# Kernel optimization log

Hardware: AMD Instinct MI355X
Metric: run time of the kernel (lower is better)

Reference implementation:

```python
import jax, jax.numpy as jnp
import numpy as np
from jax import lax

B, NQ, C = 2, 1024, 2048
H, DH = 16, 128
G, CD = 4, 512          # off_grps, off_dim = C // G
LR, HR = 24, 72         # low-res grid side, high-res grid side
INTER = 64
K = LR * LR             # sampled K/V tokens (grid_size == lr_size)


def setup_inputs() -> dict:
    key = jax.random.key(0)
    ks = jax.random.split(key, 16)
    s = 0.02
    d = {}
    d['hidden_states'] = jax.random.normal(ks[0], (B, NQ, C), jnp.float32)
    d['image_hd'] = jax.random.normal(ks[1], (B, HR * HR, C), jnp.float32)
    d['wq'] = jax.random.normal(ks[2], (C, C), jnp.float32) * s
    d['wk'] = jax.random.normal(ks[3], (C, C), jnp.float32) * s
    d['wv'] = jax.random.normal(ks[4], (C, C), jnp.float32) * s
    d['wo'] = jax.random.normal(ks[5], (C, C), jnp.float32) * s
    d['conv_dw_w'] = jax.random.normal(ks[6], (CD, 1, 3, 3), jnp.float32) * s
    d['ln1_w'] = jnp.ones((CD,), jnp.float32)
    d['ln1_b'] = jnp.zeros((CD,), jnp.float32)
    d['conv_lr_proj_w'] = jax.random.normal(ks[7], (INTER, CD), jnp.float32) * s
    d['proj_int_w'] = jax.random.normal(ks[8], (INTER, CD), jnp.float32) * s
    d['proj_int_b'] = jnp.zeros((INTER,), jnp.float32)
    d['ln2_w'] = jnp.ones((INTER,), jnp.float32)
    d['ln2_b'] = jnp.zeros((INTER,), jnp.float32)
    d['conv_off_w'] = jax.random.normal(ks[9], (2, INTER), jnp.float32) * s
    d['k_hd_w'] = jax.random.normal(ks[10], (C, C), jnp.float32) * s
    d['k_hd_b'] = jnp.zeros((C,), jnp.float32)
    d['v_hd_w'] = jax.random.normal(ks[11], (C, C), jnp.float32) * s
    d['v_hd_b'] = jnp.zeros((C,), jnp.float32)
    return d


def _ln_channels(x, w, b, eps=1e-5):
    # LayerNorm2d: normalize over channel axis of [N, C, H, W]
    mu = jnp.mean(x, axis=1, keepdims=True)
    var = jnp.var(x, axis=1, keepdims=True)
    xn = (x - mu) * lax.rsqrt(var + eps)
    return xn * w[None, :, None, None] + b[None, :, None, None]


def _tokens_to_grid(x, S):
    # [B, S*S, C] -> [B*G, CD, S, S]  (group channels like einops '(b) (h w) (g c) -> (b g) c h w')
    return x.reshape(B, S, S, G, CD).transpose(0, 3, 4, 1, 2).reshape(B * G, CD, S, S)


def _bilinear_sample(img, grid):
    # img [N, C, Hh, Wh]; grid [N, K, 2] (x, y) normalized to [-1, 1], align_corners=True
    N, Cc, Hh, Wh = img.shape
    x = (grid[..., 0] + 1.0) * 0.5 * (Wh - 1)
    y = (grid[..., 1] + 1.0) * 0.5 * (Hh - 1)
    x0f, y0f = jnp.floor(x), jnp.floor(y)
    wx = (x - x0f)[:, None, :]
    wy = (y - y0f)[:, None, :]
    x0 = jnp.clip(x0f.astype(jnp.int32), 0, Wh - 1)
    x1 = jnp.clip(x0 + 1, 0, Wh - 1)
    y0 = jnp.clip(y0f.astype(jnp.int32), 0, Hh - 1)
    y1 = jnp.clip(y0 + 1, 0, Hh - 1)
    imgf = img.reshape(N, Cc, Hh * Wh)
    gather = jax.vmap(lambda im, ix: im[:, ix])  # ([C,HW],[K]) -> [C,K]
    v00 = gather(imgf, y0 * Wh + x0)
    v01 = gather(imgf, y0 * Wh + x1)
    v10 = gather(imgf, y1 * Wh + x0)
    v11 = gather(imgf, y1 * Wh + x1)
    return (v00 * (1 - wx) * (1 - wy) + v01 * wx * (1 - wy)
            + v10 * (1 - wx) * wy + v11 * wx * wy)  # [N, C, K]


def _ref_grid():
    # normalized reference points as in _grid_generate (centers / (S-1) * 2 - 1)
    yy = (jnp.linspace(0.5, LR - 0.5, LR) / (LR - 1.0)) * 2.0 - 1.0
    xx = (jnp.linspace(0.5, LR - 0.5, LR) / (LR - 1.0)) * 2.0 - 1.0
    gy, gx = jnp.meshgrid(yy, xx, indexing='ij')
    return jnp.stack([gx, gy], axis=-1).reshape(K, 2)  # (x, y)


def reference(hidden_states, image_hd, wq, wk, wv, wo, conv_dw_w, ln1_w, ln1_b,
              conv_lr_proj_w, proj_int_w, proj_int_b, ln2_w, ln2_b, conv_off_w,
              k_hd_w, k_hd_b, v_hd_w, v_hd_b):
    # ---- QKV on the full sequence ----
    q = hidden_states @ wq.T
    k_txt = hidden_states @ wk.T
    v_txt = hidden_states @ wv.T

    # ---- offset network on LR image tokens (first LR*LR tokens) ----
    lr = _tokens_to_grid(hidden_states[:, :K, :], LR)          # [B*G, CD, LR, LR]
    x = lax.conv_general_dilated(lr, conv_dw_w, (1, 1), 'SAME',
                                 feature_group_count=CD,
                                 dimension_numbers=('NCHW', 'OIHW', 'NCHW'))
    x = jax.nn.silu(x)
    x = _ln_channels(x, ln1_w, ln1_b)
    x = jnp.einsum('nchw,oc->nohw', x, conv_lr_proj_w)          # 1x1 conv -> [B*G, INTER, LR, LR]
    # intention gate from spatially pooled group features
    pooled = jnp.mean(lr, axis=(2, 3))                          # [B*G, CD]
    gate = jax.nn.sigmoid(pooled @ proj_int_w.T + proj_int_b)   # [B*G, INTER]
    x = x * gate[:, :, None, None]
    x = _ln_channels(x, ln2_w, ln2_b)
    off = jnp.einsum('nchw,oc->nohw', x, conv_off_w)            # [B*G, 2, LR, LR]
    off = off.transpose(0, 2, 3, 1).reshape(B * G, K, 2)        # (x, y)
    pos = jnp.tanh(_ref_grid()[None] + off)                     # sampling locs in [-1, 1]

    # ---- deformable gather from HD features ----
    hd = _tokens_to_grid(image_hd, HR)                          # [B*G, CD, HR, HR]
    samp = _bilinear_sample(hd, pos)                            # [B*G, CD, K]
    samp = samp.reshape(B, G, CD, K).transpose(0, 3, 1, 2).reshape(B, K, C)
    k_hd = samp @ k_hd_w.T + k_hd_b
    v_hd = samp @ v_hd_w.T + v_hd_b

    # ---- attention: causal over text tokens, HD tokens fully visible ----
    k_all = jnp.concatenate([k_txt, k_hd], axis=1)              # [B, NQ+K, C]
    v_all = jnp.concatenate([v_txt, v_hd], axis=1)
    qh = q.reshape(B, NQ, H, DH).transpose(0, 2, 1, 3)
    kh = k_all.reshape(B, NQ + K, H, DH).transpose(0, 2, 1, 3)
    vh = v_all.reshape(B, NQ + K, H, DH).transpose(0, 2, 1, 3)
    scores = jnp.einsum('bhqd,bhkd->bhqk', qh, kh) / jnp.sqrt(jnp.float32(DH))
    col = jnp.arange(NQ + K)
    row = jnp.arange(NQ)
    allow = (col[None, :] >= NQ) | (col[None, :] <= row[:, None])
    scores = jnp.where(allow[None, None], scores, jnp.float32(-1e9))
    attn = jax.nn.softmax(scores, axis=-1)
    out = jnp.einsum('bhqk,bhkd->bhqd', attn, vh)
    out = out.transpose(0, 2, 1, 3).reshape(B, NQ, C)
    return out @ wo.T
```

## Files before the change

### kernel.cpp

```cpp
#include <hip/hip_runtime.h>

typedef unsigned short u16;
typedef unsigned int u32;
typedef __attribute__((ext_vector_type(8))) short bf8;
typedef __attribute__((ext_vector_type(4))) float f4;
typedef __attribute__((ext_vector_type(4))) unsigned short us4;

constexpr int B = 2;
constexpr int NQ = 1024;
constexpr int C = 2048;
constexpr int DH = 128;
constexpr int G = 4;
constexpr int CD = 512;
constexpr int LR = 24;
constexpr int HR = 72;
constexpr int INTER = 64;
constexpr int K = LR * LR;
constexpr int NKV = NQ + K;

#define MFMA16(a, b, c) __builtin_amdgcn_mfma_f32_16x16x32_bf16(a, b, c, 0, 0, 0)
#define GLDS(g, l)                                                         \
  __builtin_amdgcn_global_load_lds(                                        \
      (const __attribute__((address_space(1))) void*)(g),                  \
      (__attribute__((address_space(3))) void*)(l), 16, 0, 0)

__device__ __forceinline__ u16 f2bf1(float f) {
  u32 u = __float_as_uint(f);
  u32 r = (u + 0x7fffu + ((u >> 16) & 1u)) >> 16;
  return (u16)r;
}

__global__ __launch_bounds__(256) void f2bf_k7(
    const float* __restrict__ s0, const float* __restrict__ s1,
    const float* __restrict__ s2, const float* __restrict__ s3,
    const float* __restrict__ s4, const float* __restrict__ s5,
    const float* __restrict__ s6, u16* __restrict__ d0, u16* __restrict__ d1,
    u16* __restrict__ d2, u16* __restrict__ d3, u16* __restrict__ d4,
    u16* __restrict__ d5, u16* __restrict__ d6) {
  __shared__ u16 L[64][68];
  const int y = blockIdx.y;
  const float* s;
  u16* d;
  switch (y) {
    case 0: s = s0; d = d0; break;
    case 1: s = s1; d = d1; break;
    case 2: s = s2; d = d2; break;
    case 3: s = s3; d = d3; break;
    case 4: s = s4; d = d4; break;
    case 5: s = s5; d = d5; break;
    default: s = s6; d = d6; break;
  }
  const int t = threadIdx.x;
  if (y < 4) {
    const int pc = blockIdx.x;
    const int mb = pc >> 5, kb = pc & 31;
    const int rin = t >> 2, c0 = (t & 3) * 16;
    const float* src = s + (size_t)(mb * 64 + rin) * 2048 + kb * 64 + c0;
#pragma unroll
    for (int j = 0; j < 16; j += 4) {
      float4 v = *(const float4*)(src + j);
      L[rin][c0 + j] = f2bf1(v.x);
      L[rin][c0 + j + 1] = f2bf1(v.y);
      L[rin][c0 + j + 2] = f2bf1(v.z);
      L[rin][c0 + j + 3] = f2bf1(v.w);
    }
    __syncthreads();
    u16* dst = d + (size_t)pc * 4096 + t * 16;
#pragma unroll
    for (int gg = 0; gg < 2; ++gg) {
      const int g = t * 2 + gg;
      const int rh = g & 15, ks2 = (g >> 4) & 3, kc = (g >> 6) & 1, fr = g >> 7;
      const int row = fr * 16 + rh, cc = kc * 32 + ks2 * 8;
      us4 o0, o1;
      o0.x = L[row][cc];     o0.y = L[row][cc + 1];
      o0.z = L[row][cc + 2]; o0.w = L[row][cc + 3];
      o1.x = L[row][cc + 4]; o1.y = L[row][cc + 5];
      o1.z = L[row][cc + 6]; o1.w = L[row][cc + 7];
      *(us4*)(dst + gg * 8) = o0;
      *(us4*)(dst + gg * 8 + 4) = o1;
    }
  } else {
    const size_t i0 = ((size_t)blockIdx.x * 256 + t) * 16;
#pragma unroll
    for (int j = 0; j < 16; j += 4) {
      float4 v = *(const float4*)(s + i0 + j);
      us4 o;
      o.x = f2bf1(v.x); o.y = f2bf1(v.y); o.z = f2bf1(v.z); o.w = f2bf1(v.w);
      *(us4*)(d + i0 + j) = o;
    }
  }
}

#define SB()                               \
  do {                                     \
    __builtin_amdgcn_sched_barrier(0);     \
    __builtin_amdgcn_s_barrier();          \
    __builtin_amdgcn_sched_barrier(0);     \
  } while (0)
#define WVM(n) asm volatile("s_waitcnt vmcnt(" #n ")" ::: "memory")

__global__ __launch_bounds__(512, 2) void gemm_fused(
    const u16* __restrict__ Ast, const u16* __restrict__ Wq,
    const u16* __restrict__ Wk, const u16* __restrict__ Wv,
    const u16* __restrict__ samp, const u16* __restrict__ khw,
    const u16* __restrict__ vhw, const float* __restrict__ khb,
    const float* __restrict__ vhb, u16* __restrict__ outq,
    u16* __restrict__ kg, u16* __restrict__ vg) {
  __shared__ u16 As[2][4][4096];
  __shared__ u16 Bs[2][4][4096];
  const int tid = threadIdx.x, lane = tid & 63, w = tid >> 6;
  const int ks = lane >> 4, r = lane & 15;
  const int bid = blockIdx.x;

  if (bid < 192) {
    const int wm = w >> 2, wn = w & 3;
    const int swz = (bid & 7) * 24 + (bid >> 3);
    const int mt = swz / 24, nt = swz % 24;
    const u16* Wst = (nt < 8) ? Wq : (nt < 16) ? Wk : Wv;
    const int nb0 = (nt & 7) * 4;
    const int mb0 = mt * 4;

#define ST_A03(bi, kt)                                                        \
  do {                                                                        \
    GLDS(Ast + ((size_t)(mb0 + 0) * 32 + (kt)) * 4096 + tid * 8,              \
         &As[bi][0][tid * 8]);                                                \
    GLDS(Ast + ((size_t)(mb0 + 2) * 32 + (kt)) * 4096 + tid * 8,              \
         &As[bi][2][tid * 8]);                                                \
  } while (0)
#define ST_A47(bi, kt)                                                        \
  do {                                                                        \
    GLDS(Ast + ((size_t)(mb0 + 1) * 32 + (kt)) * 4096 + tid * 8,              \
         &As[bi][1][tid * 8]);                                                \
    GLDS(Ast + ((size_t)(mb0 + 3) * 32 + (kt)) * 4096 + tid * 8,              \
         &As[bi][3][tid * 8]);                                                \
  } while (0)
#define ST_B01(bi, kt)                                                        \
  do {                                                                        \
    GLDS(Wst + ((size_t)(nb0 + 0) * 32 + (kt)) * 4096 + tid * 8,              \
         &Bs[bi][0][tid * 8]);                                                \
    GLDS(Wst + ((size_t)(nb0 + 1) * 32 + (kt)) * 4096 + tid * 8,              \
         &Bs[bi][1][tid * 8]);                                                \
  } while (0)
#define ST_B23(bi, kt)                                                        \
  do {                                                                        \
    GLDS(Wst + ((size_t)(nb0 + 2) * 32 + (kt)) * 4096 + tid * 8,              \
         &Bs[bi][2][tid * 8]);                                                \
    GLDS(Wst + ((size_t)(nb0 + 3) * 32 + (kt)) * 4096 + tid * 8,              \
         &Bs[bi][3][tid * 8]);                                                \
  } while (0)
#define RD_A(dst, bi, half, kc)                                               \
  _Pragma("unroll") for (int i2 = 0; i2 < 4; ++i2) dst[i2] =                  \
      *(const bf8*)(&As[bi][wm * 2 + (half)]                                  \
                       [((i2 * 2 + (kc)) * 4 + ks) * 128 + r * 8]);
#define RD_B(dst, bi, kc)                                                     \
  _Pragma("unroll") for (int j2 = 0; j2 < 4; ++j2) dst[j2] =                  \
      *(const bf8*)(&Bs[bi][wn][((j2 * 2 + (kc)) * 4 + ks) * 128 + r * 8]);
#define MM(ACC, AF, BF)                                                       \
  do {                                                                        \
    __builtin_amdgcn_s_setprio(1);                                            \
    _Pragma("unroll") for (int i3 = 0; i3 < 4; ++i3)                          \
        _Pragma("unroll") for (int j3 = 0; j3 < 4; ++j3) ACC[i3][j3] =        \
            MFMA16(AF[i3], BF[j3], ACC[i3][j3]);                              \
    __builtin_amdgcn_s_setprio(0);                                            \
  } while (0)

    f4 accA[4][4], accB[4][4];
#pragma unroll
    for (int i = 0; i < 4; ++i)
#pragma unroll
      for (int j = 0; j < 4; ++j) {
        accA[i][j] = f4{0.f, 0.f, 0.f, 0.f};
        accB[i][j] = f4{0.f, 0.f, 0.f, 0.f};
      }
    bf8 af[4], b0[4], b1[4];

    ST_A03(0, 0); ST_B01(0, 0); ST_B23(0, 0); ST_A47(0, 0);
    ST_A03(1, 1); ST_B01(1, 1);
    WVM(6);
    SB();

    for (int t = 0; t < 32; ++t) {
      const int buf = t & 1;
      RD_A(af, buf, 0, 0);
      RD_B(b0, buf, 0);
      if (t + 1 < 32) ST_B23(buf ^ 1, t + 1);
      SB();
      MM(accA, af, b0);
      SB();
      RD_A(af, buf, 0, 1);
      RD_B(b1, buf, 1);
      if (t + 1 < 32) ST_A47(buf ^ 1, t + 1);
      SB();
      MM(accA, af, b1);
      if (t + 1 < 32) { WVM(8); } else { WVM(0); }
      SB();
      RD_A(af, buf, 1, 0);
      if (t + 2 < 32) ST_A03(buf, t + 2);
      SB();
      MM(accB, af, b0);
      SB();
      RD_A(af, buf, 1, 1);
      if (t + 2 < 32) ST_B01(buf, t + 2);
      SB();
      MM(accB, af, b1);
      if (t + 2 < 32) { WVM(6); } else if (t + 1 < 32) { WVM(2); }
      SB();
    }

#define EPI(ACC, HALF)                                                        \
  _Pragma("unroll") for (int i = 0; i < 4; ++i)                               \
      _Pragma("unroll") for (int j = 0; j < 4; ++j)                           \
          _Pragma("unroll") for (int rr = 0; rr < 4; ++rr) {                  \
    const int m = mt * 256 + wm * 128 + (HALF)*64 + i * 16 + ks * 4 + rr;     \
    const int n = nt * 256 + wn * 64 + j * 16 + r;                            \
    const float v = ACC[i][j][rr];                                            \
    const int sel = n >> 11, nn = n & 2047, hh = nn >> 7, dd = nn & 127;      \
    const int bb = m >> 10, qq = m & 1023;                                    \
    const u16 bv = f2bf1(v);                                                  \
    if (sel == 0) {                                                           \
      outq[(size_t)m * 2048 + nn] = bv;                                       \
    } else if (sel == 1) {                                                    \
      kg[(((size_t)(bb * 16 + hh) * 50 + (qq >> 5)) * 16 + (dd >> 3)) * 256 + \
         (qq & 31) * 8 + (dd & 7)] = bv;                                      \
    } else {                                                                  \
      vg[((size_t)(bb * 16 + hh) * 200 + (qq >> 3)) * 1024 + dd * 8 +         \
         (qq & 7)] = bv;                                                      \
    }                                                                         \
  }
    EPI(accA, 0)
    EPI(accB, 1)
#undef EPI
  } else {
    const int hb = bid - 192;
    const int mt = hb >> 4, nb = hb & 15;
    const int m0 = mt * 128, n0l = nb * 128;
    const int srow = lane >> 2, scol = (lane & 3) * 8;
    const int wh = w & 3;
    const int wr = wh >> 1, wc = wh & 1;
    const bool is_v = (w >= 4);
    const u16* Wp = is_v ? vhw : khw;
    const float* bias = is_v ? vhb : khb;

#define HDST(bi, k0)                                                          \
  do {                                                                        \
    GLDS(samp + (size_t)(m0 + w * 16 + srow) * 2048 + scol + (k0),            \
         &As[bi][0][w * 512 + lane * 8]);                                     \
    GLDS(Wp + (size_t)(n0l + wh * 32 + srow) * 2048 + scol + (k0),            \
         &Bs[bi][is_v ? 1 : 0][wh * 1024 + lane * 8]);                        \
    GLDS(Wp + (size_t)(n0l + wh * 32 + 16 + srow) * 2048 + scol + (k0),       \
         &Bs[bi][is_v ? 1 : 0][wh * 1024 + 512 + lane * 8]);                  \
  } while (0)

    f4 acc[4][4];
#pragma unroll
    for (int i = 0; i < 4; ++i)
#pragma unroll
      for (int j = 0; j < 4; ++j) acc[i][j] = f4{0.f, 0.f, 0.f, 0.f};
    const int koff = ks * 8;
    const int arow = wr * 64 + r, brow = wc * 64 + r;
    const u16* Wsb = &Bs[0][is_v ? 1 : 0][0] - 0;

    HDST(0, 0);
    int cur = 0;
    for (int k0 = 0; k0 < 2048; k0 += 32) {
      __syncthreads();
      if (k0 + 32 < 2048) HDST(cur ^ 1, k0 + 32);
      bf8 af2[4], bw[4];
#pragma unroll
      for (int i = 0; i < 4; ++i)
        af2[i] = *(const bf8*)(&As[cur][0][(arow + i * 16) * 32 + koff]);
#pragma unroll
      for (int j = 0; j < 4; ++j)
        bw[j] =
            *(const bf8*)(&Bs[cur][is_v ? 1 : 0][(brow + j * 16) * 32 + koff]);
#pragma unroll
      for (int i = 0; i < 4; ++i)
#pragma unroll
        for (int j = 0; j < 4; ++j)
          acc[i][j] = MFMA16(af2[i], bw[j], acc[i][j]);
      cur ^= 1;
    }
#undef HDST
    const int rbase = ks * 4;
#pragma unroll
    for (int i = 0; i < 4; ++i) {
#pragma unroll
      for (int j = 0; j < 4; ++j) {
        const int nn = n0l + wc * 64 + j * 16 + r;
        const int hh = nn >> 7, dd = nn & 127;
#pragma unroll
        for (int rr = 0; rr < 4; ++rr) {
          const int m = m0 + wr * 64 + i * 16 + rbase + rr;
          const int bb = m / 576;
          const int kv = 1024 + (m - bb * 576);
          const u16 bv = f2bf1(acc[i][j][rr] + bias[nn]);
          if (!is_v) {
            kg[(((size_t)(bb * 16 + hh) * 50 + (kv >> 5)) * 16 + (dd >> 3)) *
                   256 +
               (kv & 31) * 8 + (dd & 7)] = bv;
          } else {
            vg[((size_t)(bb * 16 + hh) * 200 + (kv >> 3)) * 1024 + dd * 8 +
               (kv & 7)] = bv;
          }
        }
      }
    }
  }
}

__global__ __launch_bounds__(256) void gemm_out(const u16* __restrict__ A,
                                                const u16* __restrict__ W0,
                                                float* __restrict__ outf) {
  __shared__ u16 As2[2][4096];
  __shared__ u16 Ws2[2][4096];
  const int tid = threadIdx.x, lane = tid & 63, w = tid >> 6;
  const int wr = w >> 1, wc = w & 1;
  const int m0 = blockIdx.y * 128, nb = blockIdx.x;
  const int n0l = nb * 128;
  f4 acc[4][4];
#pragma unroll
  for (int i = 0; i < 4; ++i)
#pragma unroll
    for (int j = 0; j < 4; ++j) acc[i][j] = f4{0.f, 0.f, 0.f, 0.f};
  const int srow = lane >> 2, scol = (lane & 3) * 8;
  const int ch0 = w * 2;
  const u16* Ab = A + (size_t)m0 * 2048 + scol;
  const u16* Wb = W0 + (size_t)n0l * 2048 + scol;
  const int koff = (lane >> 4) * 8;
  const int arow = wr * 64 + (lane & 15), brow = wc * 64 + (lane & 15);

#define GSTAGE(bi, k0)                                                        \
  do {                                                                        \
    _Pragma("unroll") for (int c = 0; c < 2; ++c) {                           \
      const int chunk = ch0 + c;                                              \
      const int row = chunk * 16 + srow;                                      \
      GLDS(Ab + (size_t)row * 2048 + (k0), &As2[bi][chunk * 512 + lane * 8]); \
      GLDS(Wb + (size_t)row * 2048 + (k0), &Ws2[bi][chunk * 512 + lane * 8]); \
    }                                                                         \
  } while (0)

  GSTAGE(0, 0);
  int cur = 0;
  for (int k0 = 0; k0 < 2048; k0 += 32) {
    __syncthreads();
    if (k0 + 32 < 2048) GSTAGE(cur ^ 1, k0 + 32);
    bf8 af2[4], bw[4];
#pragma unroll
    for (int i = 0; i < 4; ++i)
      af2[i] = *(const bf8*)(&As2[cur][(arow + i * 16) * 32 + koff]);
#pragma unroll
    for (int j = 0; j < 4; ++j)
      bw[j] = *(const bf8*)(&Ws2[cur][(brow + j * 16) * 32 + koff]);
#pragma unroll
    for (int i = 0; i < 4; ++i)
#pragma unroll
      for (int j = 0; j < 4; ++j)
        acc[i][j] = MFMA16(af2[i], bw[j], acc[i][j]);
    cur ^= 1;
  }
#undef GSTAGE
  const int rbase = (lane >> 4) * 4;
  const int cql = lane & 15;
#pragma unroll
  for (int i = 0; i < 4; ++i)
#pragma unroll
    for (int j = 0; j < 4; ++j) {
      const int n = n0l + wc * 64 + j * 16 + cql;
#pragma unroll
      for (int rr = 0; rr < 4; ++rr) {
        const int m = m0 + wr * 64 + i * 16 + rbase + rr;
        outf[(size_t)m * 2048 + n] = acc[i][j][rr];
      }
    }
}

__global__ __launch_bounds__(256) void build_lr_t(const float* __restrict__ hs,
                                                  float* __restrict__ lr) {
  __shared__ float L[32][65];
  const int bidx = blockIdx.x;
  const int n = bidx / 144;
  const int rem = bidx % 144;
  const int pb = rem / 16, cb = rem % 16;
  const int b = n >> 2, g = n & 3;
  const int p0 = pb * 64, c0 = cb * 32;
  const int t = threadIdx.x;
  const int cl = t & 31, pr = t >> 5;
#pragma unroll
  for (int it = 0; it < 8; ++it) {
    const int p = p0 + it * 8 + pr;
    L[cl][it * 8 + pr] =
        hs[((size_t)(b * 1024 + p)) * 2048 + g * 512 + c0 + cl];
  }
  __syncthreads();
  const int pl = t & 63, cr = t >> 6;
#pragma unroll
  for (int jt = 0; jt < 8; ++jt) {
    const int c = jt * 4 + cr;
    lr[((size_t)(n * 512) + c0 + c) * 576 + p0 + pl] = L[c][pl];
  }
}

__global__ __launch_bounds__(256) void pool_lr(const float* __restrict__ lr,
                                               float* __restrict__ pooled) {
  int row = (blockIdx.x * 256 + threadIdx.x) >> 6;
  int lane = threadIdx.x & 63;
  if (row >= B * G * CD) return;
  const float* p = lr + (size_t)row * K;
  float s = 0.f;
  for (int i = lane; i < K; i += 64) s += p[i];
  for (int o = 32; o; o >>= 1) s += __shfl_xor(s, o);
  if (lane == 0) pooled[row] = s * (1.f / K);
}

__global__ __launch_bounds__(256) void dwconv_silu(const float* __restrict__ lr,
                                                   const float* __restrict__ w,
                                                   float* __restrict__ x1) {
  int idx = blockIdx.x * 256 + threadIdx.x;
  if (idx >= B * G * CD * K) return;
  int p = idx % K;
  int c = (idx / K) % CD;
  int n = idx / (K * CD);
  int y = p / LR, x = p % LR;
  const float* wp = w + c * 9;
  const float* src = lr + ((size_t)n * CD + c) * K;
  float s = 0.f;
#pragma unroll
  for (int dy = -1; dy <= 1; ++dy)
#pragma unroll
    for (int dx = -1; dx <= 1; ++dx) {
      int yy = y + dy, xx = x + dx;
      if (yy < 0 || yy >= LR || xx < 0 || xx >= LR) continue;
      s += src[yy * LR + xx] * wp[(dy + 1) * 3 + dx + 1];
    }
  x1[idx] = s / (1.f + expf(-s));
}

__global__ __launch_bounds__(256) void ln_c512(float* __restrict__ x,
                                               const float* __restrict__ w,
                                               const float* __restrict__ b) {
  const int n = blockIdx.x / 9;
  const int p0 = (blockIdx.x % 9) * 64;
  const int pl = threadIdx.x & 63;
  const int cg = threadIdx.x >> 6;
  float* base = x + (size_t)n * CD * K + p0 + pl;
  float s = 0.f, ss = 0.f;
  for (int c = cg * 128; c < cg * 128 + 128; ++c) {
    float v = base[(size_t)c * K];
    s += v; ss += v * v;
  }
  __shared__ float rs[4][64], rss[4][64];
  rs[cg][pl] = s; rss[cg][pl] = ss;
  __syncthreads();
  float S = rs[0][pl] + rs[1][pl] + rs[2][pl] + rs[3][pl];
  float SS = rss[0][pl] + rss[1][pl] + rss[2][pl] + rss[3][pl];
  const float mean = S * (1.f / CD);
  const float inv = rsqrtf(SS * (1.f / CD) - mean * mean + 1e-5f);
  for (int c = cg * 128; c < cg * 128 + 128; ++c) {
    float v = base[(size_t)c * K];
    base[(size_t)c * K] = (v - mean) * inv * w[c] + b[c];
  }
}

__global__ __launch_bounds__(576) void proj64(const float* __restrict__ x1,
                                              const float* __restrict__ w,
                                              float* __restrict__ x2) {
  const int n = blockIdx.x >> 3;
  const int o0 = (blockIdx.x & 7) * 8;
  const int p = threadIdx.x;
  const float* xb = x1 + (size_t)n * CD * K + p;
  float acc[8] = {0.f, 0.f, 0.f, 0.f, 0.f, 0.f, 0.f, 0.f};
  for (int c = 0; c < CD; ++c) {
    float v = xb[(size_t)c * K];
#pragma unroll
    for (int j = 0; j < 8; ++j) acc[j] += v * w[(o0 + j) * CD + c];
  }
#pragma unroll
  for (int j = 0; j < 8; ++j)
    x2[((size_t)n * INTER + o0 + j) * K + p] = acc[j];
}

__global__ __launch_bounds__(64) void gate_k(const float* __restrict__ pooled,
                                             const float* __restrict__ w,
                                             const float* __restrict__ bias,
                                             float* __restrict__ gate) {
  int idx = blockIdx.x * 64 + threadIdx.x;
  if (idx >= B * G * INTER) return;
  int n = idx >> 6, o = idx & 63;
  const float* pb = pooled + n * CD;
  const float* wb = w + o * CD;
  float s = bias[o];
  for (int c = 0; c < CD; ++c) s += pb[c] * wb[c];
  gate[idx] = 1.f / (1.f + expf(-s));
}

__global__ __launch_bounds__(256) void ln2_off_pos(
    const float* __restrict__ x2, const float* __restrict__ gate,
    const float* __restrict__ ln2w, const float* __restrict__ ln2b,
    const float* __restrict__ offw, float* __restrict__ pos) {
  int wid = (blockIdx.x * 256 + threadIdx.x) >> 6;
  int lane = threadIdx.x & 63;
  if (wid >= B * G * K) return;
  int n = wid / K, p = wid % K;
  float v = x2[((size_t)n * INTER + lane) * K + p] * gate[n * INTER + lane];
  float s = v, ss = v * v;
  for (int o = 32; o; o >>= 1) {
    s += __shfl_xor(s, o);
    ss += __shfl_xor(ss, o);
  }
  float mean = s * (1.f / INTER);
  float var = ss * (1.f / INTER) - mean * mean;
  float xn = (v - mean) * rsqrtf(var + 1e-5f) * ln2w[lane] + ln2b[lane];
  float ox = xn * offw[lane];
  float oy = xn * offw[INTER + lane];
  for (int o = 32; o; o >>= 1) {
    ox += __shfl_xor(ox, o);
    oy += __shfl_xor(oy, o);
  }
  if (lane == 0) {
    int yi = p / LR, xi = p % LR;
    float rx = (xi + 0.5f) / 23.f * 2.f - 1.f;
    float ry = (yi + 0.5f) / 23.f * 2.f - 1.f;
    pos[((size_t)n * K + p) * 2 + 0] = tanhf(rx + ox);
    pos[((size_t)n * K + p) * 2 + 1] = tanhf(ry + oy);
  }
}

__global__ __launch_bounds__(256) void sample_k(const float* __restrict__ img,
                                                const float* __restrict__ pos,
                                                u16* __restrict__ samp) {
  const int bk = blockIdx.x;
  const int b = bk / K, k = bk % K;
  __shared__ int s_idx[G][4];
  __shared__ float s_w[G][4];
  if (threadIdx.x < G) {
    int g = threadIdx.x;
    int n = b * G + g;
    float px = pos[((size_t)n * K + k) * 2 + 0];
    float py = pos[((size_t)n * K + k) * 2 + 1];
    float x = (px + 1.f) * 0.5f * (HR - 1);
    float y = (py + 1.f) * 0.5f * (HR - 1);
    float x0f = floorf(x), y0f = floorf(y);
    float wx = x - x0f, wy = y - y0f;
    int x0 = min(max((int)x0f, 0), HR - 1);
    int x1 = min(x0 + 1, HR - 1);
    int y0 = min(max((int)y0f, 0), HR - 1);
    int y1 = min(y0 + 1, HR - 1);
    s_idx[g][0] = y0 * HR + x0;
    s_idx[g][1] = y0 * HR + x1;
    s_idx[g][2] = y1 * HR + x0;
    s_idx[g][3] = y1 * HR + x1;
    s_w[g][0] = (1.f - wx) * (1.f - wy);
    s_w[g][1] = wx * (1.f - wy);
    s_w[g][2] = (1.f - wx) * wy;
    s_w[g][3] = wx * wy;
  }
  __syncthreads();
  const float* ib = img + (size_t)b * HR * HR * C;
  u16* ob = samp + ((size_t)b * K + k) * C;
  for (int ch = threadIdx.x; ch < C; ch += 256) {
    int g = ch >> 9;
    float v = s_w[g][0] * ib[(size_t)s_idx[g][0] * C + ch] +
              s_w[g][1] * ib[(size_t)s_idx[g][1] * C + ch] +
              s_w[g][2] * ib[(size_t)s_idx[g][2] * C + ch] +
              s_w[g][3] * ib[(size_t)s_idx[g][3] * C + ch];
    ob[ch] = f2bf1(v);
  }
}

__global__ __launch_bounds__(256) void attn_part(
    const u16* __restrict__ qb, const u16* __restrict__ kg,
    const u16* __restrict__ vg, float* __restrict__ oA,
    float* __restrict__ oB, float* __restrict__ mlA,
    float* __restrict__ mlB) {
  const int i = blockIdx.x;
  const int fam = i >> 9;
  const int r9 = i & 511;
  int bh, qblk;
  if (fam == 0) {
    const int pair = r9 & 255, half = r9 >> 8;
    bh = pair & 31;
    const int q8 = pair >> 5;
    qblk = half ? (15 - q8) : q8;
  } else {
    bh = r9 & 31;
    qblk = r9 >> 5;
  }
  const int b = bh >> 4, h = bh & 15;
  const int q0 = qblk * 64;
  const int tid = threadIdx.x, lane = tid & 63, w = tid >> 6;
  const int qw = q0 + w * 16;
  const int col = lane & 15, kpart = lane >> 4, rbase = kpart * 4;
  __shared__ u16 Ks[2][4096];
  __shared__ u16 Vs[2][4096];
  __shared__ u16 Pl[4][16 * 40];
  float* oacc = fam ? oB : oA;
  float* ml = fam ? mlB : mlA;
  bf8 qf[4];
  {
    const u16* qp =
        qb + (size_t)(b * 1024 + qw + col) * 2048 + h * 128 + kpart * 8;
#pragma unroll
    for (int dc = 0; dc < 4; ++dc) qf[dc] = *(const bf8*)(qp + dc * 32);
  }
  f4 o[8];
#pragma unroll
  for (int df = 0; df < 8; ++df) o[df] = f4{0.f, 0.f, 0.f, 0.f};
  float m_r[4] = {-1e30f, -1e30f, -1e30f, -1e30f};
  float l_p[4] = {0.f, 0.f, 0.f, 0.f};
  const float scale = 0.08838834764831845f;
  const int nt = fam ? 18 : ((q0 + 64) >> 5);
  const int kvadd = fam ? 1024 : 0;
  const u16* kbh = kg + (size_t)bh * (NKV * 128);
  const u16* vbh = vg + (size_t)bh * (NKV * 128);
  u16* pw = &Pl[w][0];

#define ASTAGE(bi, kv0)                                                       \
  do {                                                                        \
    const u16* gk = kbh + (size_t)((kv0) >> 5) * 4096 + w * 1024 + lane * 8;  \
    GLDS(gk, &Ks[bi][w * 1024 + lane * 8]);                                   \
    GLDS(gk + 512, &Ks[bi][w * 1024 + 512 + lane * 8]);                       \
    const u16* gv = vbh + (size_t)((kv0) >> 3) * 1024 + w * 1024 + lane * 8;  \
    GLDS(gv, &Vs[bi][w * 1024 + lane * 8]);                                   \
    GLDS(gv + 512, &Vs[bi][w * 1024 + 512 + lane * 8]);                       \
  } while (0)

  ASTAGE(0, kvadd);
  int cur = 0;
  for (int t = 0; t < nt; ++t) {
    const int kv0 = kvadd + (t << 5);
    __syncthreads();
    if (t + 1 < nt) ASTAGE(cur ^ 1, kvadd + ((t + 1) << 5));
    const u16* ksb = &Ks[cur][0];
    const u16* vsb = &Vs[cur][0];
    f4 s0 = {0.f, 0.f, 0.f, 0.f}, s1 = {0.f, 0.f, 0.f, 0.f};
    __builtin_amdgcn_s_setprio(1);
#pragma unroll
    for (int dc = 0; dc < 4; ++dc) {
      const int dblk = dc * 4 + kpart;
      bf8 k0f = *(const bf8*)(ksb + (dblk * 32 + col) * 8);
      bf8 k1f = *(const bf8*)(ksb + (dblk * 32 + 16 + col) * 8);
      s0 = MFMA16(qf[dc], k0f, s0);
      s1 = MFMA16(qf[dc], k1f, s1);
    }
    __builtin_amdgcn_s_setprio(0);
    float sa[4], sc[4], loc[4], p0[4], p1[4];
    bool grow = false;
    const bool need_mask = (fam == 0) && (kv0 + 31 > qw);
#pragma unroll
    for (int rr = 0; rr < 4; ++rr) {
      float a = s0[rr] * scale, c2 = s1[rr] * scale;
      if (need_mask) {
        const int qg = qw + rbase + rr;
        if (kv0 + col > qg) a = -1e30f;
        if (kv0 + 16 + col > qg) c2 = -1e30f;
      }
      sa[rr] = a; sc[rr] = c2;
      loc[rr] = fmaxf(a, c2);
      grow |= (loc[rr] > m_r[rr] + 8.f);
    }
    if (__any(grow)) {
      float fr[4];
#pragma unroll
      for (int rr = 0; rr < 4; ++rr) {
        float mx = loc[rr];
        mx = fmaxf(mx, __shfl_xor(mx, 1));
        mx = fmaxf(mx, __shfl_xor(mx, 2));
        mx = fmaxf(mx, __shfl_xor(mx, 4));
        mx = fmaxf(mx, __shfl_xor(mx, 8));
        const float mn = fmaxf(m_r[rr], mx);
        fr[rr] = __expf(m_r[rr] - mn);
        m_r[rr] = mn;
        p0[rr] = __expf(sa[rr] - mn);
        p1[rr] = __expf(sc[rr] - mn);
        l_p[rr] = l_p[rr] * fr[rr] + p0[rr] + p1[rr];
      }
#pragma unroll
      for (int df = 0; df < 8; ++df) {
        o[df][0] *= fr[0]; o[df][1] *= fr[1];
        o[df][2] *= fr[2]; o[df][3] *= fr[3];
      }
    } else {
#pragma unroll
      for (int rr = 0; rr < 4; ++rr) {
        p0[rr] = __expf(sa[rr] - m_r[rr]);
        p1[rr] = __expf(sc[rr] - m_r[rr]);
        l_p[rr] += p0[rr] + p1[rr];
      }
    }
#pragma unroll
    for (int rr = 0; rr < 4; ++rr) {
      pw[(rbase + rr) * 40 + col] = f2bf1(p0[rr]);
      pw[(rbase + rr) * 40 + 16 + col] = f2bf1(p1[rr]);
    }
    bf8 pa = *(const bf8*)(pw + col * 40 + kpart * 8);
    __builtin_amdgcn_s_setprio(1);
#pragma unroll
    for (int df = 0; df < 8; ++df) {
      bf8 vf = *(const bf8*)(vsb + (kpart * 128 + df * 16 + col) * 8);
      o[df] = MFMA16(pa, vf, o[df]);
    }
    __builtin_amdgcn_s_setprio(0);
    cur ^= 1;
  }
#undef ASTAGE
  float l_r[4];
#pragma unroll
  for (int rr = 0; rr < 4; ++rr) {
    float ps = l_p[rr];
    ps += __shfl_xor(ps, 1);
    ps += __shfl_xor(ps, 2);
    ps += __shfl_xor(ps, 4);
    ps += __shfl_xor(ps, 8);
    l_r[rr] = ps;
  }
  float* orow = oacc + (size_t)(bh * 1024 + qw + rbase) * 128 + col;
#pragma unroll
  for (int df = 0; df < 8; ++df)
#pragma unroll
    for (int rr = 0; rr < 4; ++rr)
      orow[(size_t)rr * 128 + df * 16] = o[df][rr];
  if (col == 0) {
#pragma unroll
    for (int rr = 0; rr < 4; ++rr) {
      const int row = bh * 1024 + qw + rbase + rr;
      ml[row * 2] = m_r[rr];
      ml[row * 2 + 1] = l_r[rr];
    }
  }
}

__global__ __launch_bounds__(256) void attn_merge(
    const float* __restrict__ oA, const float* __restrict__ mlA,
    const float* __restrict__ oB, const float* __restrict__ mlB,
    u16* __restrict__ aob) {
  const int gid = blockIdx.x * 256 + threadIdx.x;
  const int row = gid >> 5;
  const int d0 = (gid & 31) * 4;
  const float mA = mlA[row * 2], lA = mlA[row * 2 + 1];
  const float mB = mlB[row * 2], lB = mlB[row * 2 + 1];
  const float m = fmaxf(mA, mB);
  const float wA = __expf(mA - m), wB = __expf(mB - m);
  const float inv = 1.f / (lA * wA + lB * wB);
  const f4 a = *(const f4*)(oA + (size_t)row * 128 + d0);
  const f4 c = *(const f4*)(oB + (size_t)row * 128 + d0);
  const int bh = row >> 10, q = row & 1023;
  const int bb = bh >> 4, h = bh & 15;
  u16* dst = aob + (size_t)(bb * 1024 + q) * 2048 + h * 128 + d0;
#pragma unroll
  for (int j = 0; j < 4; ++j)
    dst[j] = f2bf1((a[j] * wA + c[j] * wB) * inv);
}

extern "C" void kernel_launch(void* const* d_in, const int* in_sizes, int n_in,
                              void* d_out, int out_size, void* d_ws,
                              size_t ws_size, hipStream_t stream) {
  const float* hs = (const float*)d_in[0];
  const float* img = (const float*)d_in[1];
  const float* wq = (const float*)d_in[2];
  const float* wk = (const float*)d_in[3];
  const float* wv = (const float*)d_in[4];
  const float* wo = (const float*)d_in[5];
  const float* cdw = (const float*)d_in[6];
  const float* ln1w = (const float*)d_in[7];
  const float* ln1b = (const float*)d_in[8];
  const float* plrw = (const float*)d_in[9];
  const float* piw = (const float*)d_in[10];
  const float* pib = (const float*)d_in[11];
  const float* ln2w = (const float*)d_in[12];
  const float* ln2b = (const float*)d_in[13];
  const float* offw = (const float*)d_in[14];
  const float* khw = (const float*)d_in[15];
  const float* khb = (const float*)d_in[16];
  const float* vhw = (const float*)d_in[17];
  const float* vhb = (const float*)d_in[18];
  float* outp = (float*)d_out;

  u16* wsp = (u16*)d_ws;
  const size_t SZ = 4194304;
  u16* hs_st = wsp;
  u16* wq_st = wsp + SZ;
  u16* wk_st = wsp + 2 * SZ;
  u16* wv_st = wsp + 3 * SZ;
  u16* wo_bf = wsp + 4 * SZ;
  u16* khw_bf = wsp + 5 * SZ;
  u16* vhw_bf = wsp + 6 * SZ;
  u16* qb_bf = wsp + 7 * SZ;
  u16* samp_bf = wsp + 8 * SZ;
  u16* kg = wsp + 8 * SZ + 2359296;
  u16* vg = kg + 6553600;
  float* lrb = (float*)kg;
  float* x1b = lrb + 2359296;
  float* x2b = x1b + 2359296;
  float* poolb = x2b + 294912;
  float* gb = poolb + 4096;
  float* posb = (float*)(vg + 6553600);
  float* mlA = posb + 9216;
  float* mlB = mlA + 65536;
  float* oA = (float*)(wsp + 2 * SZ);
  float* oB = (float*)(wsp + 5 * SZ);
  u16* aob_bf = wq_st;

  dim3 blk(256);
  build_lr_t<<<dim3(1152), blk, 0, stream>>>(hs, lrb);
  pool_lr<<<dim3((B * G * CD) / 4), blk, 0, stream>>>(lrb, poolb);
  dwconv_silu<<<dim3((B * G * CD * K) / 256), blk, 0, stream>>>(lrb, cdw, x1b);
  ln_c512<<<dim3(B * G * 9), blk, 0, stream>>>(x1b, ln1w, ln1b);
  proj64<<<dim3(B * G * 8), dim3(576), 0, stream>>>(x1b, plrw, x2b);
  gate_k<<<dim3((B * G * INTER) / 64), dim3(64), 0, stream>>>(poolb, piw, pib,
                                                              gb);
  ln2_off_pos<<<dim3((B * G * K) / 4), blk, 0, stream>>>(x2b, gb, ln2w, ln2b,
                                                         offw, posb);
  sample_k<<<dim3(B * K), blk, 0, stream>>>(img, posb, samp_bf);

  f2bf_k7<<<dim3(1024, 7), blk, 0, stream>>>(hs, wq, wk, wv, wo, khw, vhw,
                                             hs_st, wq_st, wk_st, wv_st,
                                             wo_bf, khw_bf, vhw_bf);

  gemm_fused<<<dim3(336), dim3(512), 0, stream>>>(
      hs_st, wq_st, wk_st, wv_st, samp_bf, khw_bf, vhw_bf, khb, vhb, qb_bf,
      kg, vg);
  attn_part<<<dim3(1024), blk, 0, stream>>>(qb_bf, kg, vg, oA, oB, mlA, mlB);
  attn_merge<<<dim3(4096), blk, 0, stream>>>(oA, mlA, oB, mlB, aob_bf);
  gemm_out<<<dim3(16, 16), blk, 0, stream>>>(aob_bf, wo_bf, outp);
}
```

Baseline: 367.8 us.

## Fuse low-res offset branch kernels and pre-stage attention output for out-projection GEMM

Merges the LR grid transpose, mean pooling and depthwise conv+SiLU into one dwpool kernel that keeps a channel slab in LDS. It also fuses LayerNorm with the 512->64 projection, using a transposed weight produced by an extra slice of the conversion kernel. The output projection now reads wo and the attention output in the pre-tiled MFMA staging layout, written directly by attn_merge, so the GEMM loads contiguous 8KB tiles. The aim is fewer launches and less global traffic, at the cost of only 128 and 72 blocks in the fused small kernels, which may underuse the GPU.

```diff
diff --git a/kernel.cpp b/kernel.cpp
--- a/kernel.cpp
+++ b/kernel.cpp
@@ -30,15 +30,23 @@
   return (u16)r;
 }
 
-__global__ __launch_bounds__(256) void f2bf_k7(
+__global__ __launch_bounds__(256) void f2bf_k8(
     const float* __restrict__ s0, const float* __restrict__ s1,
     const float* __restrict__ s2, const float* __restrict__ s3,
     const float* __restrict__ s4, const float* __restrict__ s5,
-    const float* __restrict__ s6, u16* __restrict__ d0, u16* __restrict__ d1,
-    u16* __restrict__ d2, u16* __restrict__ d3, u16* __restrict__ d4,
-    u16* __restrict__ d5, u16* __restrict__ d6) {
+    const float* __restrict__ s6, const float* __restrict__ plrw,
+    u16* __restrict__ d0, u16* __restrict__ d1, u16* __restrict__ d2,
+    u16* __restrict__ d3, u16* __restrict__ d4, u16* __restrict__ d5,
+    u16* __restrict__ d6, float* __restrict__ wt) {
   __shared__ u16 L[64][68];
   const int y = blockIdx.y;
+  const int t = threadIdx.x;
+  if (y == 7) {
+    if (blockIdx.x >= 128) return;
+    const int idx = blockIdx.x * 256 + t;
+    wt[idx] = plrw[(idx & 63) * 512 + (idx >> 6)];
+    return;
+  }
   const float* s;
   u16* d;
   switch (y) {
@@ -50,8 +58,7 @@
     case 5: s = s5; d = d5; break;
     default: s = s6; d = d6; break;
   }
-  const int t = threadIdx.x;
-  if (y < 4) {
+  if (y < 5) {
     const int pc = blockIdx.x;
     const int mb = pc >> 5, kb = pc & 31;
     const int rin = t >> 2, c0 = (t & 3) * 16;
@@ -258,7 +265,6 @@
       for (int j = 0; j < 4; ++j) acc[i][j] = f4{0.f, 0.f, 0.f, 0.f};
     const int koff = ks * 8;
     const int arow = wr * 64 + r, brow = wc * 64 + r;
-    const u16* Wsb = &Bs[0][is_v ? 1 : 0][0] - 0;
 
     HDST(0, 0);
     int cur = 0;
@@ -308,175 +314,183 @@
   }
 }
 
-__global__ __launch_bounds__(256) void gemm_out(const u16* __restrict__ A,
-                                                const u16* __restrict__ W0,
-                                                float* __restrict__ outf) {
-  __shared__ u16 As2[2][4096];
-  __shared__ u16 Ws2[2][4096];
+__global__ __launch_bounds__(256) void gemm_out_st(const u16* __restrict__ Ast2,
+                                                   const u16* __restrict__ Wst,
+                                                   float* __restrict__ outf) {
+  __shared__ u16 As2[2][2][4096];
+  __shared__ u16 Ws2[2][2][4096];
   const int tid = threadIdx.x, lane = tid & 63, w = tid >> 6;
   const int wr = w >> 1, wc = w & 1;
-  const int m0 = blockIdx.y * 128, nb = blockIdx.x;
-  const int n0l = nb * 128;
+  const int ks = lane >> 4, r = lane & 15;
+  const int mt = blockIdx.y, nt = blockIdx.x;
+
+#define OST(bi, kt)                                                           \
+  do {                                                                        \
+    const size_t a0 = ((size_t)(mt * 2 + 0) * 32 + (kt)) * 4096;              \
+    const size_t a1 = ((size_t)(mt * 2 + 1) * 32 + (kt)) * 4096;              \
+    const size_t w0 = ((size_t)(nt * 2 + 0) * 32 + (kt)) * 4096;              \
+    const size_t w1 = ((size_t)(nt * 2 + 1) * 32 + (kt)) * 4096;              \
+    GLDS(Ast2 + a0 + tid * 8, &As2[bi][0][tid * 8]);                          \
+    GLDS(Ast2 + a0 + 2048 + tid * 8, &As2[bi][0][2048 + tid * 8]);            \
+    GLDS(Ast2 + a1 + tid * 8, &As2[bi][1][tid * 8]);                          \
+    GLDS(Ast2 + a1 + 2048 + tid * 8, &As2[bi][1][2048 + tid * 8]);            \
+    GLDS(Wst + w0 + tid * 8, &Ws2[bi][0][tid * 8]);                           \
+    GLDS(Wst + w0 + 2048 + tid * 8, &Ws2[bi][0][2048 + tid * 8]);             \
+    GLDS(Wst + w1 + tid * 8, &Ws2[bi][1][tid * 8]);                           \
+    GLDS(Wst + w1 + 2048 + tid * 8, &Ws2[bi][1][2048 + tid * 8]);             \
+  } while (0)
+
   f4 acc[4][4];
 #pragma unroll
   for (int i = 0; i < 4; ++i)
 #pragma unroll
     for (int j = 0; j < 4; ++j) acc[i][j] = f4{0.f, 0.f, 0.f, 0.f};
-  const int srow = lane >> 2, scol = (lane & 3) * 8;
-  const int ch0 = w * 2;
-  const u16* Ab = A + (size_t)m0 * 2048 + scol;
-  const u16* Wb = W0 + (size_t)n0l * 2048 + scol;
-  const int koff = (lane >> 4) * 8;
-  const int arow = wr * 64 + (lane & 15), brow = wc * 64 + (lane & 15);
-
-#define GSTAGE(bi, k0)                                                        \
-  do {                                                                        \
-    _Pragma("unroll") for (int c = 0; c < 2; ++c) {                           \
-      const int chunk = ch0 + c;                                              \
-      const int row = chunk * 16 + srow;                                      \
-      GLDS(Ab + (size_t)row * 2048 + (k0), &As2[bi][chunk * 512 + lane * 8]); \
-      GLDS(Wb + (size_t)row * 2048 + (k0), &Ws2[bi][chunk * 512 + lane * 8]); \
-    }                                                                         \
-  } while (0)
-
-  GSTAGE(0, 0);
+
+  OST(0, 0);
   int cur = 0;
-  for (int k0 = 0; k0 < 2048; k0 += 32) {
+  for (int kt = 0; kt < 32; ++kt) {
     __syncthreads();
-    if (k0 + 32 < 2048) GSTAGE(cur ^ 1, k0 + 32);
-    bf8 af2[4], bw[4];
-#pragma unroll
-    for (int i = 0; i < 4; ++i)
-      af2[i] = *(const bf8*)(&As2[cur][(arow + i * 16) * 32 + koff]);
-#pragma unroll
-    for (int j = 0; j < 4; ++j)
-      bw[j] = *(const bf8*)(&Ws2[cur][(brow + j * 16) * 32 + koff]);
-#pragma unroll
-    for (int i = 0; i < 4; ++i)
+    if (kt + 1 < 32) OST(cur ^ 1, kt + 1);
+#pragma unroll
+    for (int kc = 0; kc < 2; ++kc) {
+      bf8 a_[4], b_[4];
+#pragma unroll
+      for (int i = 0; i < 4; ++i)
+        a_[i] = *(const bf8*)(&As2[cur][wr][((i * 2 + kc) * 4 + ks) * 128 +
+                                            r * 8]);
 #pragma unroll
       for (int j = 0; j < 4; ++j)
-        acc[i][j] = MFMA16(af2[i], bw[j], acc[i][j]);
+        b_[j] = *(const bf8*)(&Ws2[cur][wc][((j * 2 + kc) * 4 + ks) * 128 +
+                                            r * 8]);
+#pragma unroll
+      for (int i = 0; i < 4; ++i)
+#pragma unroll
+        for (int j = 0; j < 4; ++j)
+          acc[i][j] = MFMA16(a_[i], b_[j], acc[i][j]);
+    }
     cur ^= 1;
   }
-#undef GSTAGE
-  const int rbase = (lane >> 4) * 4;
-  const int cql = lane & 15;
+#undef OST
 #pragma unroll
   for (int i = 0; i < 4; ++i)
 #pragma unroll
     for (int j = 0; j < 4; ++j) {
-      const int n = n0l + wc * 64 + j * 16 + cql;
+      const int n = nt * 128 + wc * 64 + j * 16 + r;
 #pragma unroll
       for (int rr = 0; rr < 4; ++rr) {
-        const int m = m0 + wr * 64 + i * 16 + rbase + rr;
+        const int m = mt * 128 + wr * 64 + i * 16 + ks * 4 + rr;
         outf[(size_t)m * 2048 + n] = acc[i][j][rr];
       }
     }
 }
 
-__global__ __launch_bounds__(256) void build_lr_t(const float* __restrict__ hs,
-                                                  float* __restrict__ lr) {
-  __shared__ float L[32][65];
+__global__ __launch_bounds__(256) void dwpool(const float* __restrict__ hs,
+                                              const float* __restrict__ cw,
+                                              float* __restrict__ x1,
+                                              float* __restrict__ pooled) {
+  __shared__ float L[32][577];
   const int bidx = blockIdx.x;
-  const int n = bidx / 144;
-  const int rem = bidx % 144;
-  const int pb = rem / 16, cb = rem % 16;
+  const int n = bidx >> 4, cg = bidx & 15;
   const int b = n >> 2, g = n & 3;
-  const int p0 = pb * 64, c0 = cb * 32;
+  const int c0 = cg * 32;
   const int t = threadIdx.x;
-  const int cl = t & 31, pr = t >> 5;
-#pragma unroll
-  for (int it = 0; it < 8; ++it) {
-    const int p = p0 + it * 8 + pr;
-    L[cl][it * 8 + pr] =
-        hs[((size_t)(b * 1024 + p)) * 2048 + g * 512 + c0 + cl];
+  {
+    const int c = t & 31, pr = t >> 5;
+    const float* src = hs + (size_t)b * 1024 * 2048 + g * 512 + c0 + c;
+#pragma unroll 4
+    for (int j = 0; j < 72; ++j) {
+      const int p = j * 8 + pr;
+      L[c][p] = src[(size_t)p * 2048];
+    }
   }
   __syncthreads();
-  const int pl = t & 63, cr = t >> 6;
-#pragma unroll
-  for (int jt = 0; jt < 8; ++jt) {
-    const int c = jt * 4 + cr;
-    lr[((size_t)(n * 512) + c0 + c) * 576 + p0 + pl] = L[c][pl];
-  }
-}
-
-__global__ __launch_bounds__(256) void pool_lr(const float* __restrict__ lr,
-                                               float* __restrict__ pooled) {
-  int row = (blockIdx.x * 256 + threadIdx.x) >> 6;
-  int lane = threadIdx.x & 63;
-  if (row >= B * G * CD) return;
-  const float* p = lr + (size_t)row * K;
-  float s = 0.f;
-  for (int i = lane; i < K; i += 64) s += p[i];
-  for (int o = 32; o; o >>= 1) s += __shfl_xor(s, o);
-  if (lane == 0) pooled[row] = s * (1.f / K);
-}
-
-__global__ __launch_bounds__(256) void dwconv_silu(const float* __restrict__ lr,
-                                                   const float* __restrict__ w,
-                                                   float* __restrict__ x1) {
-  int idx = blockIdx.x * 256 + threadIdx.x;
-  if (idx >= B * G * CD * K) return;
-  int p = idx % K;
-  int c = (idx / K) % CD;
-  int n = idx / (K * CD);
-  int y = p / LR, x = p % LR;
-  const float* wp = w + c * 9;
-  const float* src = lr + ((size_t)n * CD + c) * K;
-  float s = 0.f;
-#pragma unroll
-  for (int dy = -1; dy <= 1; ++dy)
-#pragma unroll
-    for (int dx = -1; dx <= 1; ++dx) {
-      int yy = y + dy, xx = x + dx;
-      if (yy < 0 || yy >= LR || xx < 0 || xx >= LR) continue;
-      s += src[yy * LR + xx] * wp[(dy + 1) * 3 + dx + 1];
-    }
-  x1[idx] = s / (1.f + expf(-s));
-}
-
-__global__ __launch_bounds__(256) void ln_c512(float* __restrict__ x,
-                                               const float* __restrict__ w,
-                                               const float* __restrict__ b) {
-  const int n = blockIdx.x / 9;
-  const int p0 = (blockIdx.x % 9) * 64;
-  const int pl = threadIdx.x & 63;
-  const int cg = threadIdx.x >> 6;
-  float* base = x + (size_t)n * CD * K + p0 + pl;
-  float s = 0.f, ss = 0.f;
-  for (int c = cg * 128; c < cg * 128 + 128; ++c) {
-    float v = base[(size_t)c * K];
-    s += v; ss += v * v;
-  }
+  {
+    const int c = t >> 3, seg = t & 7;
+    float s = 0.f;
+    for (int i = 0; i < 72; ++i) s += L[c][seg * 72 + i];
+    s += __shfl_xor(s, 1);
+    s += __shfl_xor(s, 2);
+    s += __shfl_xor(s, 4);
+    if (seg == 0) pooled[n * 512 + c0 + c] = s * (1.f / 576.f);
+  }
+  const size_t base_out = (size_t)(n * 512 + c0) * 576;
+  for (int j = 0; j < 72; ++j) {
+    const int idx = j * 256 + t;
+    const int c = idx / 576, p = idx - c * 576;
+    const int y = p / 24, x = p - y * 24;
+    const float* wp = cw + (c0 + c) * 9;
+    float s = 0.f;
+#pragma unroll
+    for (int dy = -1; dy <= 1; ++dy)
+#pragma unroll
+      for (int dx = -1; dx <= 1; ++dx) {
+        const int yy = y + dy, xx = x + dx;
+        if (yy < 0 || yy >= 24 || xx < 0 || xx >= 24) continue;
+        s += L[c][yy * 24 + xx] * wp[(dy + 1) * 3 + dx + 1];
+      }
+    x1[base_out + idx] = s / (1.f + expf(-s));
+  }
+}
+
+__global__ __launch_bounds__(256) void lnproj(const float* __restrict__ x1,
+                                              const float* __restrict__ ln1w,
+                                              const float* __restrict__ ln1b,
+                                              const float* __restrict__ wt,
+                                              float* __restrict__ x2) {
+  __shared__ float Xs[512][68];
   __shared__ float rs[4][64], rss[4][64];
-  rs[cg][pl] = s; rss[cg][pl] = ss;
+  const int bidx = blockIdx.x;
+  const int n = bidx / 9, pc = bidx % 9;
+  const int p0 = pc * 64;
+  const int t = threadIdx.x;
+  {
+    const int pl = t & 63, c4 = t >> 6;
+    const float* src = x1 + (size_t)n * 512 * 576 + p0 + pl;
+#pragma unroll 4
+    for (int j = 0; j < 128; ++j) {
+      const int c = j * 4 + c4;
+      Xs[c][pl] = src[(size_t)c * 576];
+    }
+  }
   __syncthreads();
-  float S = rs[0][pl] + rs[1][pl] + rs[2][pl] + rs[3][pl];
-  float SS = rss[0][pl] + rss[1][pl] + rss[2][pl] + rss[3][pl];
-  const float mean = S * (1.f / CD);
-  const float inv = rsqrtf(SS * (1.f / CD) - mean * mean + 1e-5f);
-  for (int c = cg * 128; c < cg * 128 + 128; ++c) {
-    float v = base[(size_t)c * K];
-    base[(size_t)c * K] = (v - mean) * inv * w[c] + b[c];
-  }
-}
-
-__global__ __launch_bounds__(576) void proj64(const float* __restrict__ x1,
-                                              const float* __restrict__ w,
-                                              float* __restrict__ x2) {
-  const int n = blockIdx.x >> 3;
-  const int o0 = (blockIdx.x & 7) * 8;
-  const int p = threadIdx.x;
-  const float* xb = x1 + (size_t)n * CD * K + p;
-  float acc[8] = {0.f, 0.f, 0.f, 0.f, 0.f, 0.f, 0.f, 0.f};
-  for (int c = 0; c < CD; ++c) {
-    float v = xb[(size_t)c * K];
-#pragma unroll
-    for (int j = 0; j < 8; ++j) acc[j] += v * w[(o0 + j) * CD + c];
-  }
-#pragma unroll
-  for (int j = 0; j < 8; ++j)
-    x2[((size_t)n * INTER + o0 + j) * K + p] = acc[j];
+  {
+    const int pl = t & 63, q = t >> 6;
+    float s = 0.f, ss = 0.f;
+    for (int c = q * 128; c < q * 128 + 128; ++c) {
+      const float v = Xs[c][pl];
+      s += v;
+      ss += v * v;
+    }
+    rs[q][pl] = s;
+    rss[q][pl] = ss;
+    __syncthreads();
+    const float S = rs[0][pl] + rs[1][pl] + rs[2][pl] + rs[3][pl];
+    const float SS = rss[0][pl] + rss[1][pl] + rss[2][pl] + rss[3][pl];
+    const float mean = S * (1.f / 512.f);
+    const float inv = rsqrtf(SS * (1.f / 512.f) - mean * mean + 1e-5f);
+    for (int c = q * 128; c < q * 128 + 128; ++c)
+      Xs[c][pl] = (Xs[c][pl] - mean) * inv * ln1w[c] + ln1b[c];
+  }
+  __syncthreads();
+  {
+    const int o4 = (t & 15) * 4, pl0 = (t >> 4) * 4;
+    float acc[4][4] = {};
+    for (int c = 0; c < 512; ++c) {
+      const f4 xv = *(const f4*)(&Xs[c][pl0]);
+      const f4 wv = *(const f4*)(&wt[c * 64 + o4]);
+#pragma unroll
+      for (int i = 0; i < 4; ++i)
+#pragma unroll
+        for (int j = 0; j < 4; ++j) acc[i][j] += wv[i] * xv[j];
+    }
+#pragma unroll
+    for (int i = 0; i < 4; ++i) {
+      f4 ov;
+      ov[0] = acc[i][0]; ov[1] = acc[i][1];
+      ov[2] = acc[i][2]; ov[3] = acc[i][3];
+      *(f4*)(&x2[(size_t)(n * 64 + o4 + i) * 576 + p0 + pl0]) = ov;
+    }
+  }
 }
 
 __global__ __launch_bounds__(64) void gate_k(const float* __restrict__ pooled,
@@ -732,7 +746,7 @@
 __global__ __launch_bounds__(256) void attn_merge(
     const float* __restrict__ oA, const float* __restrict__ mlA,
     const float* __restrict__ oB, const float* __restrict__ mlB,
-    u16* __restrict__ aob) {
+    u16* __restrict__ aob_st) {
   const int gid = blockIdx.x * 256 + threadIdx.x;
   const int row = gid >> 5;
   const int d0 = (gid & 31) * 4;
@@ -745,10 +759,19 @@
   const f4 c = *(const f4*)(oB + (size_t)row * 128 + d0);
   const int bh = row >> 10, q = row & 1023;
   const int bb = bh >> 4, h = bh & 15;
-  u16* dst = aob + (size_t)(bb * 1024 + q) * 2048 + h * 128 + d0;
-#pragma unroll
-  for (int j = 0; j < 4; ++j)
-    dst[j] = f2bf1((a[j] * wA + c[j] * wB) * inv);
+  const int mm = bb * 1024 + q;
+  const int col = h * 128 + d0;
+  const int mb = mm >> 6, fr = (mm >> 4) & 3, r = mm & 15;
+  const int kb = col >> 6, kc = (col >> 5) & 1, ks = (col >> 3) & 3,
+            j0 = col & 7;
+  u16* dst = aob_st + ((size_t)(mb * 32 + kb)) * 4096 +
+             (((fr * 2 + kc) * 4 + ks) * 16 + r) * 8 + j0;
+  us4 ov;
+  ov.x = f2bf1((a[0] * wA + c[0] * wB) * inv);
+  ov.y = f2bf1((a[1] * wA + c[1] * wB) * inv);
+  ov.z = f2bf1((a[2] * wA + c[2] * wB) * inv);
+  ov.w = f2bf1((a[3] * wA + c[3] * wB) * inv);
+  *(us4*)dst = ov;
 }
 
 extern "C" void kernel_launch(void* const* d_in, const int* in_sizes, int n_in,
@@ -781,45 +804,39 @@
   u16* wq_st = wsp + SZ;
   u16* wk_st = wsp + 2 * SZ;
   u16* wv_st = wsp + 3 * SZ;
-  u16* wo_bf = wsp + 4 * SZ;
+  u16* wo_st = wsp + 4 * SZ;
   u16* khw_bf = wsp + 5 * SZ;
   u16* vhw_bf = wsp + 6 * SZ;
   u16* qb_bf = wsp + 7 * SZ;
   u16* samp_bf = wsp + 8 * SZ;
   u16* kg = wsp + 8 * SZ + 2359296;
   u16* vg = kg + 6553600;
-  float* lrb = (float*)kg;
-  float* x1b = lrb + 2359296;
+  float* x1b = (float*)kg + 2359296;
   float* x2b = x1b + 2359296;
   float* poolb = x2b + 294912;
   float* gb = poolb + 4096;
   float* posb = (float*)(vg + 6553600);
   float* mlA = posb + 9216;
   float* mlB = mlA + 65536;
+  float* wtb = mlB + 65536;
   float* oA = (float*)(wsp + 2 * SZ);
   float* oB = (float*)(wsp + 5 * SZ);
-  u16* aob_bf = wq_st;
+  u16* aob_st = wq_st;
 
   dim3 blk(256);
-  build_lr_t<<<dim3(1152), blk, 0, stream>>>(hs, lrb);
-  pool_lr<<<dim3((B * G * CD) / 4), blk, 0, stream>>>(lrb, poolb);
-  dwconv_silu<<<dim3((B * G * CD * K) / 256), blk, 0, stream>>>(lrb, cdw, x1b);
-  ln_c512<<<dim3(B * G * 9), blk, 0, stream>>>(x1b, ln1w, ln1b);
-  proj64<<<dim3(B * G * 8), dim3(576), 0, stream>>>(x1b, plrw, x2b);
-  gate_k<<<dim3((B * G * INTER) / 64), dim3(64), 0, stream>>>(poolb, piw, pib,
-                                                              gb);
-  ln2_off_pos<<<dim3((B * G * K) / 4), blk, 0, stream>>>(x2b, gb, ln2w, ln2b,
-                                                         offw, posb);
+  dwpool<<<dim3(128), blk, 0, stream>>>(hs, cdw, x1b, poolb);
+  f2bf_k8<<<dim3(1024, 8), blk, 0, stream>>>(hs, wq, wk, wv, wo, khw, vhw,
+                                             plrw, hs_st, wq_st, wk_st, wv_st,
+                                             wo_st, khw_bf, vhw_bf, wtb);
+  lnproj<<<dim3(72), blk, 0, stream>>>(x1b, ln1w, ln1b, wtb, x2b);
+  gate_k<<<dim3(8), dim3(64), 0, stream>>>(poolb, piw, pib, gb);
+  ln2_off_pos<<<dim3(1152), blk, 0, stream>>>(x2b, gb, ln2w, ln2b, offw, posb);
   sample_k<<<dim3(B * K), blk, 0, stream>>>(img, posb, samp_bf);
-
-  f2bf_k7<<<dim3(1024, 7), blk, 0, stream>>>(hs, wq, wk, wv, wo, khw, vhw,
-                                             hs_st, wq_st, wk_st, wv_st,
-                                             wo_bf, khw_bf, vhw_bf);
 
   gemm_fused<<<dim3(336), dim3(512), 0, stream>>>(
       hs_st, wq_st, wk_st, wv_st, samp_bf, khw_bf, vhw_bf, khb, vhb, qb_bf,
       kg, vg);
   attn_part<<<dim3(1024), blk, 0, stream>>>(qb_bf, kg, vg, oA, oB, mlA, mlB);
-  attn_merge<<<dim3(4096), blk, 0, stream>>>(oA, mlA, oB, mlB, aob_bf);
-  gemm_out<<<dim3(16, 16), blk, 0, stream>>>(aob_bf, wo_bf, outp);
-}
+  attn_merge<<<dim3(4096), blk, 0, stream>>>(oA, mlA, oB, mlB, aob_st);
+  gemm_out_st<<<dim3(16, 16), blk, 0, stream>>>(aob_st, wo_st, outp);
+}
```

Measured after the change: 367.8 us. Within noise of the previous version (-0.0%).
